# Kernel tuning notes

Measured on AMD Instinct MI355X. Metric: run time of the kernel, lower is better.

## Reference

```python
import jax, jax.numpy as jnp
import numpy as np

EPS = 1e-08


def setup_inputs() -> dict:
    key = jax.random.key(0)
    X = jax.random.normal(key, (16384, 768), dtype=jnp.float32)
    return {"X": X}


def reference(X) -> jnp.ndarray:
    # L2-normalize rows (torch F.normalize with eps: divide by max(norm, eps))
    norms = jnp.linalg.norm(X, axis=-1, keepdims=True)
    Xn = X / jnp.maximum(norms, EPS)

    n = Xn.shape[0]
    # pairwise inner products [n, n]; mask self-similarity on diagonal with -1
    dots = Xn @ Xn.T
    dots = jnp.where(jnp.eye(n, dtype=bool), jnp.float32(-1.0), dots)
    I = jnp.argmax(dots, axis=1)  # nearest neighbor index per row

    # torch PairwiseDistance(2, eps): ||x - y + eps||_2
    diff = Xn - Xn[I] + EPS
    distances = jnp.linalg.norm(diff, axis=-1)

    # loss_type == 'standard'
    loss = -jnp.mean(jnp.log(distances + EPS))
    return loss
```

## Files before the change

kernel.cpp:

```cpp
#include <hip/hip_runtime.h>
#include <hip/hip_bf16.h>
#include <stdint.h>
#include <math.h>

#define NR 16384
#define DIM 768
#define KEPS 1e-8f

#define BM 128
#define BK 64
#define NB (NR / BM)
#define KT (DIM / BK)
#define NTILES (NB * (NB + 1) / 2)

typedef __attribute__((ext_vector_type(4))) float f32x4;
typedef __attribute__((ext_vector_type(2))) long long2_t;

__device__ inline uint32_t fkey(float f) {
    union { float f; uint32_t u; } v; v.f = f;
    return (v.u & 0x80000000u) ? ~v.u : (v.u | 0x80000000u);
}

__device__ inline unsigned long long pack_vc(float v, int c) {
    return ((unsigned long long)fkey(v) << 32) | (unsigned)c;
}

__device__ inline void gload16(const uint8_t* g, const uint8_t* l) {
    __builtin_amdgcn_global_load_lds(
        (const __attribute__((address_space(1))) void*)g,
        (__attribute__((address_space(3))) void*)l,
        16, 0, 0);
}

__device__ inline uint8_t f2fp8(float f) {
    union { float f; uint32_t u; } v; v.f = f;
    const uint8_t s = (uint8_t)((v.u >> 24) & 0x80u);
    float a = fabsf(f);
    if (a >= 448.0f) return s | 0x7E;
    if (a < 0.015625f) {
        int q = (int)rintf(a * 512.0f);
        if (q >= 8) return s | 0x08;
        return s | (uint8_t)q;
    }
    int ex; float m = frexpf(a, &ex);
    int E = ex + 6;
    int frac = (int)rintf(m * 16.0f - 8.0f);
    if (frac >= 8) { frac = 0; ++E; if (E > 15) return s | 0x7E; }
    return s | (uint8_t)(E << 3) | (uint8_t)frac;
}

__global__ __launch_bounds__(256) void k_norm(const float* __restrict__ X,
                                              uint8_t* __restrict__ Xn,
                                              float* __restrict__ norms) {
    __shared__ uint8_t buf[4][768];
    const int wid = threadIdx.x >> 6, lane = threadIdx.x & 63;
    const int row = blockIdx.x * 4 + wid;
    const float4* xr = (const float4*)(X + (size_t)row * DIM) + lane * 3;
    float4 a = xr[0], b = xr[1], c = xr[2];
    float s = a.x*a.x + a.y*a.y + a.z*a.z + a.w*a.w
            + b.x*b.x + b.y*b.y + b.z*b.z + b.w*b.w
            + c.x*c.x + c.y*c.y + c.z*c.z + c.w*c.w;
#pragma unroll
    for (int m = 32; m >= 1; m >>= 1) s += __shfl_xor(s, m);
    const float n = sqrtf(s);
    if (lane == 0) norms[row] = n;
    const float rn = 1.0f / fmaxf(n, KEPS);
    float v[12] = {a.x,a.y,a.z,a.w,b.x,b.y,b.z,b.w,c.x,c.y,c.z,c.w};
    uint8_t q[12];
#pragma unroll
    for (int i = 0; i < 12; ++i) q[i] = f2fp8(v[i] * rn);
    uint32_t* lb = (uint32_t*)&buf[wid][lane * 12];
    lb[0] = (uint32_t)q[0] | ((uint32_t)q[1] << 8) | ((uint32_t)q[2]  << 16) | ((uint32_t)q[3]  << 24);
    lb[1] = (uint32_t)q[4] | ((uint32_t)q[5] << 8) | ((uint32_t)q[6]  << 16) | ((uint32_t)q[7]  << 24);
    lb[2] = (uint32_t)q[8] | ((uint32_t)q[9] << 8) | ((uint32_t)q[10] << 16) | ((uint32_t)q[11] << 24);
    __syncthreads();
    if (lane < 48) {
        const int blk = lane >> 2;
        const int h   = lane & 3;
        const uint2 lo = *(const uint2*)&buf[wid][blk * 64 + h * 8];
        const uint2 hi = *(const uint2*)&buf[wid][blk * 64 + 32 + h * 8];
        *(uint4*)(Xn + (size_t)row * DIM + lane * 16) = make_uint4(lo.x, lo.y, hi.x, hi.y);
    }
}

__global__ __launch_bounds__(256) void k_init(unsigned long long* __restrict__ nn64) {
    nn64[blockIdx.x * 256 + threadIdx.x] = pack_vc(-2.0f, 0);
}

__global__ __launch_bounds__(256, 4) void k_maxdot(const uint8_t* __restrict__ Xn,
                                                   unsigned long long* __restrict__ nn64) {
    __shared__ uint8_t lA[BM * BK];
    __shared__ uint8_t lB[BM * BK];
    const int tid  = threadIdx.x;
    const int lane = tid & 63, wid = tid >> 6;
    const int wr = wid >> 1, wc = wid & 1;
    const int l15 = lane & 15, lhi = lane >> 4;

    int t = (int)blockIdx.x;
    t = (t & 7) * (NTILES / 8) + (t >> 3);
    float disc = 66049.0f - 8.0f * (float)t;
    int rb = (int)((257.0f - sqrtf(disc)) * 0.5f);
    if (rb > NB - 1) rb = NB - 1;
    if (rb < 0) rb = 0;
    while (rb > 0 && rb * (257 - rb) / 2 > t) --rb;
    while ((rb + 1) * (257 - (rb + 1)) / 2 <= t) ++rb;
    const int cb = rb + (t - rb * (257 - rb) / 2);
    const int rowbase = rb * BM;
    const int colbase = cb * BM;
    const bool diag = (rb == cb);

    f32x4 acc[4][4];
    const f32x4 z = {0.f, 0.f, 0.f, 0.f};
#pragma unroll
    for (int i = 0; i < 4; ++i)
#pragma unroll
        for (int j = 0; j < 4; ++j) acc[i][j] = z;

    const int s_r0 = tid >> 2;
    const int s_c  = tid & 3;

    for (int kt = 0; kt < KT; ++kt) {
#pragma unroll
        for (int it = 0; it < 2; ++it) {
            const int r = it * 64 + s_r0;
            const int c = s_c ^ ((r >> 1) & 3);
            const size_t koff = (size_t)kt * BK + c * 16;
            gload16(Xn + (size_t)(rowbase + r) * DIM + koff, lA + it * 4096 + wid * 1024);
            gload16(Xn + (size_t)(colbase + r) * DIM + koff, lB + it * 4096 + wid * 1024);
        }
        __syncthreads();
        long2_t afp[4], bgp[4];
#pragma unroll
        for (int mf = 0; mf < 4; ++mf) {
            const int r = wr * 64 + mf * 16 + l15;
            afp[mf] = *(const long2_t*)(lA + r * 64 + ((lhi ^ ((r >> 1) & 3)) << 4));
        }
#pragma unroll
        for (int nf = 0; nf < 4; ++nf) {
            const int r = wc * 64 + nf * 16 + l15;
            bgp[nf] = *(const long2_t*)(lB + r * 64 + ((lhi ^ ((r >> 1) & 3)) << 4));
        }
#pragma unroll
        for (int mf = 0; mf < 4; ++mf)
#pragma unroll
            for (int nf = 0; nf < 4; ++nf)
                acc[mf][nf] = __builtin_amdgcn_mfma_f32_16x16x32_fp8_fp8(
                    afp[mf].x, bgp[nf].x, acc[mf][nf], 0, 0, 0);
#pragma unroll
        for (int mf = 0; mf < 4; ++mf)
#pragma unroll
            for (int nf = 0; nf < 4; ++nf)
                acc[mf][nf] = __builtin_amdgcn_mfma_f32_16x16x32_fp8_fp8(
                    afp[mf].y, bgp[nf].y, acc[mf][nf], 0, 0, 0);
        __syncthreads();
    }

    if (diag) {
#pragma unroll
        for (int mf = 0; mf < 4; ++mf)
#pragma unroll
            for (int nf = 0; nf < 4; ++nf)
#pragma unroll
                for (int rr = 0; rr < 4; ++rr) {
                    const int rl = wr * 64 + mf * 16 + lhi * 4 + rr;
                    const int cl = wc * 64 + nf * 16 + l15;
                    if (rl == cl) acc[mf][nf][rr] = -1.0f;
                }
    }

#pragma unroll
    for (int mf = 0; mf < 4; ++mf)
#pragma unroll
        for (int rr = 0; rr < 4; ++rr) {
            float v = acc[mf][0][rr];
            int   c = colbase + wc * 64 + l15;
#pragma unroll
            for (int nf = 1; nf < 4; ++nf) {
                const float w2 = acc[mf][nf][rr];
                const int   c2 = colbase + wc * 64 + nf * 16 + l15;
                if (w2 > v) { v = w2; c = c2; }
            }
#pragma unroll
            for (int m = 1; m <= 8; m <<= 1) {
                const float ov = __shfl_xor(v, m);
                const int   oc = __shfl_xor(c, m);
                if (ov > v) { v = ov; c = oc; }
            }
            if (l15 == 0) {
                const int r = rowbase + wr * 64 + mf * 16 + lhi * 4 + rr;
                atomicMax(&nn64[r], pack_vc(v, c));
            }
        }

#pragma unroll
    for (int nf = 0; nf < 4; ++nf) {
        float v = acc[0][nf][0];
        int   c = rowbase + wr * 64 + lhi * 4;
#pragma unroll
        for (int mf = 0; mf < 4; ++mf)
#pragma unroll
            for (int rr = 0; rr < 4; ++rr) {
                if (mf == 0 && rr == 0) continue;
                const float w2 = acc[mf][nf][rr];
                const int   c2 = rowbase + wr * 64 + mf * 16 + lhi * 4 + rr;
                if (w2 > v) { v = w2; c = c2; }
            }
#pragma unroll
        for (int m = 16; m <= 32; m <<= 1) {
            const float ov = __shfl_xor(v, m);
            const int   oc = __shfl_xor(c, m);
            if (ov > v) { v = ov; c = oc; }
        }
        if ((lane >> 4) == 0) {
            const int cc = colbase + wc * 64 + nf * 16 + l15;
            atomicMax(&nn64[cc], pack_vc(v, c));
        }
    }
}

__global__ __launch_bounds__(256) void k_refine(const float* __restrict__ X,
                                                const float* __restrict__ norms,
                                                const unsigned long long* __restrict__ nn64,
                                                float* __restrict__ logd) {
    const int wid = threadIdx.x >> 6, lane = threadIdx.x & 63;
    const int r = blockIdx.x * 4 + wid;
    const int j = (int)(nn64[r] & 0xFFFFu);
    const float rnr = 1.0f / fmaxf(norms[r], KEPS);
    const float rnj = 1.0f / fmaxf(norms[j], KEPS);
    const float4* xr = (const float4*)(X + (size_t)r * DIM) + lane * 3;
    const float4* xj = (const float4*)(X + (size_t)j * DIM) + lane * 3;
    float s = 0.0f;
#pragma unroll
    for (int i = 0; i < 3; ++i) {
        const float4 a = xr[i], b = xj[i];
        float d;
        d = a.x * rnr - b.x * rnj + KEPS; s = fmaf(d, d, s);
        d = a.y * rnr - b.y * rnj + KEPS; s = fmaf(d, d, s);
        d = a.z * rnr - b.z * rnj + KEPS; s = fmaf(d, d, s);
        d = a.w * rnr - b.w * rnj + KEPS; s = fmaf(d, d, s);
    }
#pragma unroll
    for (int m = 32; m >= 1; m >>= 1) s += __shfl_xor(s, m);
    if (lane == 0) logd[r] = logf(sqrtf(s) + KEPS);
}

__global__ __launch_bounds__(256) void k_loss(const float* __restrict__ logd,
                                              float* __restrict__ out) {
    float local = 0.0f;
    for (int r = threadIdx.x; r < NR; r += 256) local += logd[r];
#pragma unroll
    for (int m = 32; m >= 1; m >>= 1) local += __shfl_xor(local, m);
    __shared__ float red[4];
    const int lane = threadIdx.x & 63, wid = threadIdx.x >> 6;
    if (lane == 0) red[wid] = local;
    __syncthreads();
    if (threadIdx.x == 0)
        out[0] = -(red[0] + red[1] + red[2] + red[3]) / (float)NR;
}

extern "C" void kernel_launch(void* const* d_in, const int* in_sizes, int n_in,
                              void* d_out, int out_size, void* d_ws, size_t ws_size,
                              hipStream_t stream) {
    const float* X = (const float*)d_in[0];
    float* out = (float*)d_out;
    uint8_t* Xn = (uint8_t*)d_ws;
    char* p = (char*)d_ws + (size_t)NR * DIM;
    float* norms = (float*)p;                 p += (size_t)NR * 4;
    unsigned long long* nn64 = (unsigned long long*)p; p += (size_t)NR * 8;
    float* logd = (float*)p;

    k_norm<<<NR / 4, 256, 0, stream>>>(X, Xn, norms);
    k_init<<<NR / 256, 256, 0, stream>>>(nn64);
    k_maxdot<<<NTILES, 256, 0, stream>>>(Xn, nn64);
    k_refine<<<NR / 4, 256, 0, stream>>>(X, norms, nn64, logd);
    k_loss<<<1, 256, 0, stream>>>(logd, out);
}
```

Before: 311.8 us.

## Store FP8 rows in tiled-transposed layout and load MFMA fragments directly from global

```diff
diff --git a/kernel.cpp b/kernel.cpp
--- a/kernel.cpp
+++ b/kernel.cpp
@@ -8,9 +8,9 @@
 #define KEPS 1e-8f
 
 #define BM 128
-#define BK 64
 #define NB (NR / BM)
-#define KT (DIM / BK)
+#define KT (DIM / 64)
+#define NQ (DIM / 16)
 #define NTILES (NB * (NB + 1) / 2)
 
 typedef __attribute__((ext_vector_type(4))) float f32x4;
@@ -23,13 +23,6 @@
 
 __device__ inline unsigned long long pack_vc(float v, int c) {
     return ((unsigned long long)fkey(v) << 32) | (unsigned)c;
-}
-
-__device__ inline void gload16(const uint8_t* g, const uint8_t* l) {
-    __builtin_amdgcn_global_load_lds(
-        (const __attribute__((address_space(1))) void*)g,
-        (__attribute__((address_space(3))) void*)l,
-        16, 0, 0);
 }
 
 __device__ inline uint8_t f2fp8(float f) {
@@ -50,7 +43,7 @@
 }
 
 __global__ __launch_bounds__(256) void k_norm(const float* __restrict__ X,
-                                              uint8_t* __restrict__ Xn,
+                                              uint8_t* __restrict__ XnT,
                                               float* __restrict__ norms) {
     __shared__ uint8_t buf[4][768];
     const int wid = threadIdx.x >> 6, lane = threadIdx.x & 63;
@@ -74,12 +67,14 @@
     lb[1] = (uint32_t)q[4] | ((uint32_t)q[5] << 8) | ((uint32_t)q[6]  << 16) | ((uint32_t)q[7]  << 24);
     lb[2] = (uint32_t)q[8] | ((uint32_t)q[9] << 8) | ((uint32_t)q[10] << 16) | ((uint32_t)q[11] << 24);
     __syncthreads();
-    if (lane < 48) {
+    if (lane < NQ) {
         const int blk = lane >> 2;
         const int h   = lane & 3;
         const uint2 lo = *(const uint2*)&buf[wid][blk * 64 + h * 8];
         const uint2 hi = *(const uint2*)&buf[wid][blk * 64 + 32 + h * 8];
-        *(uint4*)(Xn + (size_t)row * DIM + lane * 16) = make_uint4(lo.x, lo.y, hi.x, hi.y);
+        const size_t off = ((size_t)(row >> 7) * NQ * 128 + (size_t)lane * 128
+                            + (row & 127)) * 16;
+        *(uint4*)(XnT + off) = make_uint4(lo.x, lo.y, hi.x, hi.y);
     }
 }
 
@@ -87,10 +82,8 @@
     nn64[blockIdx.x * 256 + threadIdx.x] = pack_vc(-2.0f, 0);
 }
 
-__global__ __launch_bounds__(256, 4) void k_maxdot(const uint8_t* __restrict__ Xn,
+__global__ __launch_bounds__(256, 3) void k_maxdot(const uint8_t* __restrict__ XnT,
                                                    unsigned long long* __restrict__ nn64) {
-    __shared__ uint8_t lA[BM * BK];
-    __shared__ uint8_t lB[BM * BK];
     const int tid  = threadIdx.x;
     const int lane = tid & 63, wid = tid >> 6;
     const int wr = wid >> 1, wc = wid & 1;
@@ -109,6 +102,9 @@
     const int colbase = cb * BM;
     const bool diag = (rb == cb);
 
+    const uint8_t* pA = XnT + (size_t)rb * NQ * 128 * 16;
+    const uint8_t* pB = XnT + (size_t)cb * NQ * 128 * 16;
+
     f32x4 acc[4][4];
     const f32x4 z = {0.f, 0.f, 0.f, 0.f};
 #pragma unroll
@@ -116,43 +112,30 @@
 #pragma unroll
         for (int j = 0; j < 4; ++j) acc[i][j] = z;
 
-    const int s_r0 = tid >> 2;
-    const int s_c  = tid & 3;
-
+    const int arow = wr * 64 + l15;
+    const int brow = wc * 64 + l15;
+#pragma unroll 2
     for (int kt = 0; kt < KT; ++kt) {
-#pragma unroll
-        for (int it = 0; it < 2; ++it) {
-            const int r = it * 64 + s_r0;
-            const int c = s_c ^ ((r >> 1) & 3);
-            const size_t koff = (size_t)kt * BK + c * 16;
-            gload16(Xn + (size_t)(rowbase + r) * DIM + koff, lA + it * 4096 + wid * 1024);
-            gload16(Xn + (size_t)(colbase + r) * DIM + koff, lB + it * 4096 + wid * 1024);
-        }
-        __syncthreads();
-        long2_t afp[4], bgp[4];
-#pragma unroll
-        for (int mf = 0; mf < 4; ++mf) {
-            const int r = wr * 64 + mf * 16 + l15;
-            afp[mf] = *(const long2_t*)(lA + r * 64 + ((lhi ^ ((r >> 1) & 3)) << 4));
-        }
-#pragma unroll
-        for (int nf = 0; nf < 4; ++nf) {
-            const int r = wc * 64 + nf * 16 + l15;
-            bgp[nf] = *(const long2_t*)(lB + r * 64 + ((lhi ^ ((r >> 1) & 3)) << 4));
-        }
+        const size_t qoff = (size_t)(kt * 4 + lhi) * 128 * 16;
+        long2_t af[4], bg[4];
+#pragma unroll
+        for (int mf = 0; mf < 4; ++mf)
+            af[mf] = *(const long2_t*)(pA + qoff + (size_t)(arow + mf * 16) * 16);
+#pragma unroll
+        for (int nf = 0; nf < 4; ++nf)
+            bg[nf] = *(const long2_t*)(pB + qoff + (size_t)(brow + nf * 16) * 16);
 #pragma unroll
         for (int mf = 0; mf < 4; ++mf)
 #pragma unroll
             for (int nf = 0; nf < 4; ++nf)
                 acc[mf][nf] = __builtin_amdgcn_mfma_f32_16x16x32_fp8_fp8(
-                    afp[mf].x, bgp[nf].x, acc[mf][nf], 0, 0, 0);
+                    af[mf].x, bg[nf].x, acc[mf][nf], 0, 0, 0);
 #pragma unroll
         for (int mf = 0; mf < 4; ++mf)
 #pragma unroll
             for (int nf = 0; nf < 4; ++nf)
                 acc[mf][nf] = __builtin_amdgcn_mfma_f32_16x16x32_fp8_fp8(
-                    afp[mf].y, bgp[nf].y, acc[mf][nf], 0, 0, 0);
-        __syncthreads();
+                    af[mf].y, bg[nf].y, acc[mf][nf], 0, 0, 0);
     }
 
     if (diag) {
@@ -263,15 +246,15 @@
                               hipStream_t stream) {
     const float* X = (const float*)d_in[0];
     float* out = (float*)d_out;
-    uint8_t* Xn = (uint8_t*)d_ws;
+    uint8_t* XnT = (uint8_t*)d_ws;
     char* p = (char*)d_ws + (size_t)NR * DIM;
     float* norms = (float*)p;                 p += (size_t)NR * 4;
     unsigned long long* nn64 = (unsigned long long*)p; p += (size_t)NR * 8;
     float* logd = (float*)p;
 
-    k_norm<<<NR / 4, 256, 0, stream>>>(X, Xn, norms);
+    k_norm<<<NR / 4, 256, 0, stream>>>(X, XnT, norms);
     k_init<<<NR / 256, 256, 0, stream>>>(nn64);
-    k_maxdot<<<NTILES, 256, 0, stream>>>(Xn, nn64);
+    k_maxdot<<<NTILES, 256, 0, stream>>>(XnT, nn64);
     k_refine<<<NR / 4, 256, 0, stream>>>(X, norms, nn64, logd);
     k_loss<<<1, 256, 0, stream>>>(logd, out);
 }
```

Result: no change. 307.9 us (-1.3%).
